# Performance work log

Measured on AMD Instinct MI355X. Metric: run time of the kernel, lower is better.

Reference implementation:

```python
import jax, jax.numpy as jnp
import numpy as np

B, T, E, H = 2, 2048, 1024, 16
HD = E // H
EPS = 1e-5


def layer_norm(x, g, b):
    mu = jnp.mean(x, axis=-1, keepdims=True)
    var = jnp.mean(jnp.square(x - mu), axis=-1, keepdims=True)
    return (x - mu) * jax.lax.rsqrt(var + EPS) * g + b


def setup_inputs() -> dict:
    key = jax.random.key(0)
    ks = jax.random.split(key, 12)
    s = 0.02
    return {
        "x": jax.random.normal(ks[0], (B, T, E), jnp.float32),
        "Wk": jax.random.normal(ks[1], (E, E), jnp.float32) * s,
        "Wq": jax.random.normal(ks[2], (E, E), jnp.float32) * s,
        "Wv": jax.random.normal(ks[3], (E, E), jnp.float32) * s,
        "Wp": jax.random.normal(ks[4], (E, E), jnp.float32) * s,
        "bp": jnp.zeros((E,), jnp.float32),
        "W1": jax.random.normal(ks[5], (E, 4 * E), jnp.float32) * s,
        "b1": jnp.zeros((4 * E,), jnp.float32),
        "W2": jax.random.normal(ks[6], (4 * E, E), jnp.float32) * s,
        "b2": jnp.zeros((E,), jnp.float32),
        "g1": jnp.ones((E,), jnp.float32),
        "be1": jnp.zeros((E,), jnp.float32),
        "g2": jnp.ones((E,), jnp.float32),
        "be2": jnp.zeros((E,), jnp.float32),
    }


def reference(x, Wk, Wq, Wv, Wp, bp, W1, b1, W2, b2, g1, be1, g2, be2):
    # --- attention sublayer ---
    h = layer_norm(x, g1, be1)
    q = (h @ Wq).reshape(B, T, H, HD).transpose(0, 2, 1, 3)  # [B,H,T,HD]
    k = (h @ Wk).reshape(B, T, H, HD).transpose(0, 2, 1, 3)
    v = (h @ Wv).reshape(B, T, H, HD).transpose(0, 2, 1, 3)
    scores = jnp.einsum('bhqd,bhkd->bhqk', q, k) * (HD ** -0.5)
    causal = jnp.tril(jnp.ones((T, T), bool))
    scores = jnp.where(causal, scores, -jnp.inf)
    probs = jax.nn.softmax(scores, axis=-1)  # dropout is identity (eval)
    attn = jnp.einsum('bhqk,bhkd->bhqd', probs, v)
    attn = attn.transpose(0, 2, 1, 3).reshape(B, T, E)
    x = x + attn @ Wp + bp
    # --- FFN sublayer ---
    h2 = layer_norm(x, g2, be2)
    ff = jax.nn.relu(h2 @ W1 + b1) @ W2 + b2
    return x + ff
```

## Files before the change

kernel.cpp:

```cpp
#include <hip/hip_runtime.h>
#include <hip/hip_bf16.h>

#define B_ 2
#define T_ 2048
#define E_ 1024
#define H_ 16
#define HD_ 64
#define NT (B_*T_)

typedef __attribute__((ext_vector_type(8))) short s16x8;
typedef __attribute__((ext_vector_type(4))) float f32x4;

using bf16 = __hip_bfloat16;

#define MFMA16(a,b,c) __builtin_amdgcn_mfma_f32_16x16x32_bf16(a,b,c,0,0,0)

__device__ inline unsigned short f2bf(float f) {
    bf16 h = __float2bfloat16(f);
    return *reinterpret_cast<unsigned short*>(&h);
}

__device__ __forceinline__ unsigned cvt_pk_bf16(float lo, float hi) {
    unsigned r;
    asm("v_cvt_pk_bf16_f32 %0, %1, %2" : "=v"(r) : "v"(lo), "v"(hi));
    return r;
}

__device__ __forceinline__ float exp2_fast(float x) {
    float r;
    asm("v_exp_f32 %0, %1" : "=v"(r) : "v"(x));
    return r;
}

__device__ __forceinline__ void async_cp16(const void* g, void* l) {
    __builtin_amdgcn_global_load_lds((const __attribute__((address_space(1))) void*)g,
                                     (__attribute__((address_space(3))) void*)l,
                                     16, 0, 0);
}

__global__ __launch_bounds__(256) void transpose_all(const float* __restrict__ Wq,
                                                     const float* __restrict__ Wk,
                                                     const float* __restrict__ Wv,
                                                     const float* __restrict__ Wp,
                                                     const float* __restrict__ W1,
                                                     const float* __restrict__ W2,
                                                     bf16* __restrict__ Wqkv_t,
                                                     bf16* __restrict__ W1_t,
                                                     bf16* __restrict__ W2_t) {
    __shared__ float tile[32][33];
    int id = blockIdx.x;
    const float* src; bf16* dst; int K, N, n0, k0;
    float scl = 1.0f;
    if (id < 4096) {
        int z = id >> 10, t = id & 1023;
        src = z == 0 ? Wq : z == 1 ? Wk : z == 2 ? Wv : Wp;
        if (z == 0) scl = 0.125f * 1.44269504088896f;
        dst = Wqkv_t + (size_t)z * 1048576;
        K = 1024; N = 1024; n0 = (t & 31) * 32; k0 = (t >> 5) * 32;
    } else if (id < 8192) {
        int t = id - 4096; src = W1; dst = W1_t; K = 1024; N = 4096;
        n0 = (t & 127) * 32; k0 = (t >> 7) * 32;
    } else {
        int t = id - 8192; src = W2; dst = W2_t; K = 4096; N = 1024;
        n0 = (t & 31) * 32; k0 = (t >> 5) * 32;
    }
    int tx = threadIdx.x, ty = threadIdx.y;
#pragma unroll
    for (int i = 0; i < 4; ++i)
        tile[ty + i*8][tx] = src[(size_t)(k0 + ty + i*8)*N + n0 + tx];
    __syncthreads();
#pragma unroll
    for (int i = 0; i < 4; ++i)
        dst[(size_t)(n0 + ty + i*8)*K + k0 + tx] = __float2bfloat16(tile[tx][ty + i*8] * scl);
}

__global__ __launch_bounds__(256) void ln_kernel(const float* __restrict__ x,
                                                 const float* __restrict__ g,
                                                 const float* __restrict__ b,
                                                 bf16* __restrict__ h) {
    int row = blockIdx.x;
    int tid = threadIdx.x;
    const float4 xv = *reinterpret_cast<const float4*>(x + (size_t)row*E_ + tid*4);
    float s  = xv.x + xv.y + xv.z + xv.w;
    float sq = xv.x*xv.x + xv.y*xv.y + xv.z*xv.z + xv.w*xv.w;
#pragma unroll
    for (int o = 32; o > 0; o >>= 1) { s += __shfl_xor(s, o); sq += __shfl_xor(sq, o); }
    __shared__ float red[8];
    int w = tid >> 6, lane = tid & 63;
    if (lane == 0) { red[w] = s; red[4 + w] = sq; }
    __syncthreads();
    float S = red[0] + red[1] + red[2] + red[3];
    float Q = red[4] + red[5] + red[6] + red[7];
    float mu = S * (1.0f/E_);
    float var = Q * (1.0f/E_) - mu*mu;
    float rs = rsqrtf(var + 1e-5f);
    const float4 gv = *reinterpret_cast<const float4*>(g + tid*4);
    const float4 bv = *reinterpret_cast<const float4*>(b + tid*4);
    ushort4 o4;
    o4.x = f2bf((xv.x - mu)*rs*gv.x + bv.x);
    o4.y = f2bf((xv.y - mu)*rs*gv.y + bv.y);
    o4.z = f2bf((xv.z - mu)*rs*gv.z + bv.z);
    o4.w = f2bf((xv.w - mu)*rs*gv.w + bv.w);
    *reinterpret_cast<ushort4*>(h + (size_t)row*E_ + tid*4) = o4;
}

#define RD(p) (*reinterpret_cast<const s16x8*>(p))
#define MM(m,n) do { acc[m][n] = MFMA16(af[m][0], bfr[n][0], acc[m][n]); \
                     acc[m][n] = MFMA16(af[m][1], bfr[n][1], acc[m][n]); } while (0)
#define MFMAS_0 MM(0,0); MM(1,0);
#define MFMAS_1 MM(2,0); MM(3,0); MM(2,1); MM(3,1); MM(0,1); MM(1,1);
#define MFMAS_2 MM(4,0); MM(5,0); MM(4,1); MM(5,1); MM(4,2); MM(5,2); \
                MM(0,2); MM(1,2); MM(2,2); MM(3,2);
#define MFMAS_3 MM(6,0); MM(7,0); MM(6,1); MM(7,1); MM(6,2); MM(7,2); \
                MM(6,3); MM(7,3); MM(0,3); MM(1,3); MM(2,3); MM(3,3); \
                MM(4,3); MM(5,3);

template<int EPI>
__global__ __launch_bounds__(512)
void gemm8p(const bf16* __restrict__ A, const bf16* __restrict__ Bt, void* Cout,
            const float* __restrict__ bias, int M, int N, int K) {
    __shared__ char smem[131072];
    int tid = threadIdx.x;
    int lane = tid & 63, w = tid >> 6;
    int wm = w >> 2, wn = w & 3;
    int nbx = gridDim.x;
    int hid = blockIdx.y * nbx + blockIdx.x;
    int cpx = (nbx * gridDim.y) >> 3;
    int nid = (hid & 7) * cpx + (hid >> 3);
    int m0 = (nid / nbx) * 256, n0 = (nid % nbx) * 256;
    int lr = lane & 15, lq = lane >> 4;
    f32x4 acc[8][4] = {};
    int srow = tid >> 3;
    int schunk = ((tid & 7) ^ (srow & 7)) * 8;
    const bf16* ApS = A  + (size_t)(m0 + srow)*K + schunk;
    const bf16* BpS = Bt + (size_t)(n0 + srow)*K + schunk;
    int sw4 = (lr & 7) << 4;
    int x0 = (lq*16) ^ sw4, x1 = (64 + lq*16) ^ sw4;
    int aoff[8], boff[4];
#pragma unroll
    for (int m = 0; m < 8; ++m)
        aoff[m] = ((m >> 1)*64 + wm*32 + (m & 1)*16 + lr) * 128;
#pragma unroll
    for (int n = 0; n < 4; ++n)
        boff[n] = (n*64 + wn*16 + lr) * 128;
    int nst = K >> 6;
    s16x8 af[8][2], bfr[4][2];
#pragma unroll
    for (int q = 0; q < 4; ++q) {
        async_cp16(ApS + (size_t)(q*64)*K, smem + q*8192 + w*1024);
        async_cp16(BpS + (size_t)(q*64)*K, smem + 32768 + q*8192 + w*1024);
    }
    ApS += 64; BpS += 64;
    asm volatile("s_waitcnt vmcnt(6)" ::: "memory");
    __builtin_amdgcn_sched_barrier(0);
    __builtin_amdgcn_s_barrier();
    __builtin_amdgcn_sched_barrier(0);

#define PHASE(Q) do {                                                              \
    af[2*Q][0]   = RD(bufA + aoff[2*Q]   + x0);                                    \
    af[2*Q][1]   = RD(bufA + aoff[2*Q]   + x1);                                    \
    af[2*Q+1][0] = RD(bufA + aoff[2*Q+1] + x0);                                    \
    af[2*Q+1][1] = RD(bufA + aoff[2*Q+1] + x1);                                    \
    bfr[Q][0]    = RD(bufB + boff[Q] + x0);                                        \
    bfr[Q][1]    = RD(bufB + boff[Q] + x1);                                        \
    if (more) {                                                                    \
        async_cp16(ApS + (size_t)(Q*64)*K, stA + Q*8192 + w*1024);                 \
        async_cp16(BpS + (size_t)(Q*64)*K, stA + 32768 + Q*8192 + w*1024);         \
        asm volatile("s_waitcnt vmcnt(6)" ::: "memory");                           \
    } else {                                                                       \
        if (Q == 0) asm volatile("s_waitcnt vmcnt(4)" ::: "memory");               \
        else if (Q == 1) asm volatile("s_waitcnt vmcnt(2)" ::: "memory");          \
        else if (Q == 2) asm volatile("s_waitcnt vmcnt(0)" ::: "memory");          \
    }                                                                              \
    __builtin_amdgcn_sched_barrier(0);                                             \
    __builtin_amdgcn_s_barrier();                                                  \
    __builtin_amdgcn_sched_barrier(0);                                             \
    asm volatile("s_waitcnt lgkmcnt(0)" ::: "memory");                             \
    __builtin_amdgcn_sched_barrier(0);                                             \
    __builtin_amdgcn_s_setprio(1);                                                 \
    MFMAS_##Q                                                                      \
    __builtin_amdgcn_s_setprio(0);                                                 \
    __builtin_amdgcn_sched_barrier(0);                                             \
    __builtin_amdgcn_s_barrier();                                                  \
    __builtin_amdgcn_sched_barrier(0);                                             \
} while (0)

    for (int t = 0; t < nst; ++t) {
        const char* bufA = smem + (size_t)(t & 1)*65536;
        const char* bufB = bufA + 32768;
        char* stA = smem + (size_t)((t & 1) ^ 1)*65536;
        bool more = (t + 1 < nst);
        PHASE(0);
        PHASE(1);
        PHASE(2);
        PHASE(3);
        ApS += 64; BpS += 64;
    }
#undef PHASE
#pragma unroll
    for (int m = 0; m < 8; ++m) {
#pragma unroll
        for (int n = 0; n < 4; ++n) {
            int col = n0 + n*64 + wn*16 + lr;
#pragma unroll
            for (int r = 0; r < 4; ++r) {
                int row = m0 + (m >> 1)*64 + wm*32 + (m & 1)*16 + lq*4 + r;
                float v = acc[m][n][r];
                if (EPI == 0) {
                    reinterpret_cast<bf16*>(Cout)[(size_t)row*N + col] = __float2bfloat16(v);
                } else {
                    v += bias[col];
                    v = v > 0.f ? v : 0.f;
                    reinterpret_cast<bf16*>(Cout)[(size_t)row*N + col] = __float2bfloat16(v);
                }
            }
        }
    }
}

template<int BM, int BN, int EPI>
__global__ __launch_bounds__(256)
void gemm_t(const bf16* __restrict__ A, const bf16* __restrict__ Bt, void* Cout,
            const float* __restrict__ bias, const float* res,
            int M, int N, int K) {
    constexpr int MT = BM / 32;
    constexpr int NB = BN / 32;
    constexpr int MHALF = BM / 2, NHALF = BN / 2;
    __shared__ bf16 As[BM*64];
    __shared__ bf16 Bs[BN*64];
    int tid = threadIdx.x;
    int lane = tid & 63, w = tid >> 6;
    int wr = w >> 1, wc = w & 1;
    int nbx = gridDim.x;
    int hid = blockIdx.y * nbx + blockIdx.x;
    int cpx = (nbx * gridDim.y) >> 3;
    int nid = (hid & 7) * cpx + (hid >> 3);
    int m0 = (nid / nbx) * BM, n0 = (nid % nbx) * BN;
    int lr = lane & 15, lq = lane >> 4;
    f32x4 acc[MT][NB] = {};
    int srow = w*8 + (lane >> 3);
    int schunk = ((lane & 7) ^ (srow & 7)) * 8;
    const bf16* Ap = A  + (size_t)(m0 + srow)*K + schunk;
    const bf16* Bp = Bt + (size_t)(n0 + srow)*K + schunk;
    for (int k0 = 0; k0 < K; k0 += 64) {
#pragma unroll
        for (int i = 0; i < BM/32; ++i)
            async_cp16(Ap + (size_t)(i*32)*K + k0, (char*)As + i*4096 + w*1024);
#pragma unroll
        for (int i = 0; i < BN/32; ++i)
            async_cp16(Bp + (size_t)(i*32)*K + k0, (char*)Bs + i*4096 + w*1024);
        __syncthreads();
        const char* Asb = (const char*)As;
        const char* Bsb = (const char*)Bs;
        s16x8 af[2][MT], bfr[2][NB];
#pragma unroll
        for (int m = 0; m < MT; ++m) {
            int row = wr*MHALF + m*16 + lr;
            int base = row*128, sw = (row & 7) << 4;
#pragma unroll
            for (int kk = 0; kk < 2; ++kk)
                af[kk][m] = *reinterpret_cast<const s16x8*>(Asb + base + ((kk*64 + lq*16) ^ sw));
        }
#pragma unroll
        for (int n = 0; n < NB; ++n) {
            int row = wc*NHALF + n*16 + lr;
            int base = row*128, sw = (row & 7) << 4;
#pragma unroll
            for (int kk = 0; kk < 2; ++kk)
                bfr[kk][n] = *reinterpret_cast<const s16x8*>(Bsb + base + ((kk*64 + lq*16) ^ sw));
        }
        __builtin_amdgcn_s_setprio(1);
#pragma unroll
        for (int kk = 0; kk < 2; ++kk)
#pragma unroll
            for (int m = 0; m < MT; ++m)
#pragma unroll
                for (int n = 0; n < NB; ++n)
                    acc[m][n] = MFMA16(af[kk][m], bfr[kk][n], acc[m][n]);
        __builtin_amdgcn_s_setprio(0);
        __syncthreads();
    }
#pragma unroll
    for (int m = 0; m < MT; ++m) {
#pragma unroll
        for (int n = 0; n < NB; ++n) {
            int col = n0 + wc*NHALF + n*16 + lr;
#pragma unroll
            for (int r = 0; r < 4; ++r) {
                int row = m0 + wr*MHALF + m*16 + lq*4 + r;
                float v = acc[m][n][r];
                if (EPI == 0) {
                    reinterpret_cast<bf16*>(Cout)[(size_t)row*N + col] = __float2bfloat16(v);
                } else if (EPI == 1) {
                    reinterpret_cast<float*>(Cout)[(size_t)row*N + col] =
                        v + bias[col] + res[(size_t)row*N + col];
                } else {
                    v += bias[col];
                    v = v > 0.f ? v : 0.f;
                    reinterpret_cast<bf16*>(Cout)[(size_t)row*N + col] = __float2bfloat16(v);
                }
            }
        }
    }
}

__global__ __launch_bounds__(256) void v_transpose(const bf16* __restrict__ qkv,
                                                   bf16* __restrict__ Vt) {
    __shared__ unsigned short tile[32][33];
    int tx = threadIdx.x, ty = threadIdx.y;
    int bh = blockIdx.z;
    int b = bh >> 4, h = bh & 15;
    int t0 = blockIdx.x * 32, d0 = blockIdx.y * 32;
    const unsigned short* src = reinterpret_cast<const unsigned short*>(qkv);
#pragma unroll
    for (int i = 0; i < 4; ++i)
        tile[ty + i*8][tx] = src[(size_t)(b*T_ + t0 + ty + i*8)*3072 + 2048 + h*64 + d0 + tx];
    __syncthreads();
    unsigned short* dst = reinterpret_cast<unsigned short*>(Vt);
#pragma unroll
    for (int i = 0; i < 4; ++i)
        dst[(size_t)(bh*64 + d0 + ty + i*8)*T_ + t0 + tx] = tile[tx][ty + i*8];
}

__global__ __launch_bounds__(256)
void flash_attn(const bf16* __restrict__ qkv, const bf16* __restrict__ Vt,
                bf16* __restrict__ O) {
    __shared__ char smem[40960];
    int tid = threadIdx.x;
    int lane = tid & 63, w = tid >> 6;
    int lr = lane & 15, lq = lane >> 4;
    int bh = blockIdx.y, b = bh >> 4, h = bh & 15;
    int pm = (bh & 15) ^ ((bh & 16) ? 31 : 0);
    int qt = (int)(blockIdx.x ^ pm) & 31;
    int q0 = qt * 64;
    int qw = q0 + w * 16;
    const bf16* Qb = qkv + (size_t)(b*T_)*3072 + h*HD_;
    const bf16* Kb = Qb + 1024;
    const bf16* Vb = Vt + (size_t)bh * HD_ * T_;
    char* Pw = smem + 32768 + w*2048;

    int srow_ = w*8 + (lane >> 3);
    int sc_   = (((lane & 7) ^ (srow_ & 7))) * 8;
    const bf16* kS0 = Kb + (size_t)srow_*3072 + sc_;
    const bf16* kS1 = kS0 + (size_t)32*3072;
    const bf16* vS0 = Vb + (size_t)srow_*2048 + sc_;
    const bf16* vS1 = vS0 + (size_t)32*2048;
    char* kD = smem + w*1024;
    char* vD = smem + 16384 + w*1024;

    int sw4 = (lr & 7) << 4;
    int kvo[4], pwo[4];
#pragma unroll
    for (int n = 0; n < 4; ++n) {
        kvo[n] = n*2048 + lr*128 + ((lq << 4) ^ sw4);
        pwo[n] = (lr*128 + n*32 + lq*8) ^ sw4;
    }
    int pao0 = (lr*128 + lq*16) ^ sw4;
    int pao1 = (lr*128 + 64 + lq*16) ^ sw4;

    s16x8 qf[2];
#pragma unroll
    for (int kk = 0; kk < 2; ++kk)
        qf[kk] = *reinterpret_cast<const s16x8*>(Qb + (size_t)(qw + lr)*3072 + kk*32 + lq*8);
    f32x4 od[4] = {};
    const f32x4 Z4 = {0.f, 0.f, 0.f, 0.f};
    float lrun = 0.f;
    int ntiles = qt + 1;

    auto stageNext = [&](int bufi) {
        async_cp16(kS0, kD + bufi*8192);
        async_cp16(kS1, kD + bufi*8192 + 4096);
        async_cp16(vS0, vD + bufi*8192);
        async_cp16(vS1, vD + bufi*8192 + 4096);
        kS0 += 64*3072; kS1 += 64*3072; vS0 += 64; vS1 += 64;
    };

    auto step = [&](const char* Kt, const char* Vtl, bool diag, int kv0) {
        f32x4 sc[4];
        __builtin_amdgcn_s_setprio(1);
#pragma unroll
        for (int n = 0; n < 4; ++n) {
            s16x8 kf0 = *reinterpret_cast<const s16x8*>(Kt + kvo[n]);
            s16x8 kf1 = *reinterpret_cast<const s16x8*>(Kt + (kvo[n] ^ 64));
            f32x4 z = MFMA16(kf0, qf[0], Z4);
            z = MFMA16(kf1, qf[1], z);
            sc[n] = z;
        }
        __builtin_amdgcn_s_setprio(0);
        if (diag) {
            int q = qw + lr;
#pragma unroll
            for (int n = 0; n < 4; ++n)
#pragma unroll
                for (int r = 0; r < 4; ++r)
                    if (kv0 + n*16 + lq*4 + r > q) sc[n][r] = -1e30f;
        }
        float psum = 0.f;
#pragma unroll
        for (int n = 0; n < 4; ++n) {
            float p0 = exp2_fast(sc[n][0]);
            float p1 = exp2_fast(sc[n][1]);
            float p2 = exp2_fast(sc[n][2]);
            float p3 = exp2_fast(sc[n][3]);
            psum += (p0 + p1) + (p2 + p3);
            uint2 pk;
            pk.x = cvt_pk_bf16(p0, p1);
            pk.y = cvt_pk_bf16(p2, p3);
            *reinterpret_cast<uint2*>(Pw + pwo[n]) = pk;
        }
        psum += __shfl_xor(psum, 16);
        psum += __shfl_xor(psum, 32);
        lrun += psum;
        asm volatile("" ::: "memory");
        s16x8 pa0 = *reinterpret_cast<const s16x8*>(Pw + pao0);
        s16x8 pa1 = *reinterpret_cast<const s16x8*>(Pw + pao1);
        __builtin_amdgcn_s_setprio(1);
#pragma unroll
        for (int nd = 0; nd < 4; ++nd) {
            s16x8 vf0 = *reinterpret_cast<const s16x8*>(Vtl + kvo[nd]);
            s16x8 vf1 = *reinterpret_cast<const s16x8*>(Vtl + (kvo[nd] ^ 64));
            od[nd] = MFMA16(pa0, vf0, od[nd]);
            od[nd] = MFMA16(pa1, vf1, od[nd]);
        }
        __builtin_amdgcn_s_setprio(0);
    };

    stageNext(0);
    for (int it = 0; it < ntiles - 1; ++it) {
        int curb = it & 1;
        stageNext(curb ^ 1);
        asm volatile("s_waitcnt vmcnt(4)" ::: "memory");
        __builtin_amdgcn_sched_barrier(0);
        __builtin_amdgcn_s_barrier();
        __builtin_amdgcn_sched_barrier(0);
        step(smem + curb*8192, smem + 16384 + curb*8192, false, 0);
        __builtin_amdgcn_sched_barrier(0);
        __builtin_amdgcn_s_barrier();
        __builtin_amdgcn_sched_barrier(0);
    }
    {
        int curb = (ntiles - 1) & 1;
        asm volatile("s_waitcnt vmcnt(0)" ::: "memory");
        __builtin_amdgcn_sched_barrier(0);
        __builtin_amdgcn_s_barrier();
        __builtin_amdgcn_sched_barrier(0);
        step(smem + curb*8192, smem + 16384 + curb*8192, true, (ntiles - 1) * 64);
    }
    float lR[4];
#pragma unroll
    for (int r = 0; r < 4; ++r) lR[r] = 1.0f / __shfl(lrun, lq*4 + r);
#pragma unroll
    for (int nd = 0; nd < 4; ++nd) {
#pragma unroll
        for (int r = 0; r < 4; ++r) {
            int row = qw + lq*4 + r;
            O[(size_t)(b*T_ + row)*E_ + h*HD_ + nd*16 + lr] = __float2bfloat16(od[nd][r] * lR[r]);
        }
    }
}

extern "C" void kernel_launch(void* const* d_in, const int* in_sizes, int n_in,
                              void* d_out, int out_size, void* d_ws, size_t ws_size,
                              hipStream_t stream) {
    const float* x   = (const float*)d_in[0];
    const float* Wk  = (const float*)d_in[1];
    const float* Wq  = (const float*)d_in[2];
    const float* Wv  = (const float*)d_in[3];
    const float* Wp  = (const float*)d_in[4];
    const float* bp  = (const float*)d_in[5];
    const float* W1  = (const float*)d_in[6];
    const float* b1  = (const float*)d_in[7];
    const float* W2  = (const float*)d_in[8];
    const float* b2  = (const float*)d_in[9];
    const float* g1  = (const float*)d_in[10];
    const float* be1 = (const float*)d_in[11];
    const float* g2  = (const float*)d_in[12];
    const float* be2 = (const float*)d_in[13];
    float* out = (float*)d_out;

    char* ws = (char*)d_ws;
    bf16* Wqkv_t = (bf16*)(ws + 0);
    bf16* Wp_t   = (bf16*)(ws + 6291456);
    bf16* W1_t   = (bf16*)(ws + 8388608);
    bf16* W2_t   = (bf16*)(ws + 16777216);
    bf16* h      = (bf16*)(ws + 25165824);
    bf16* qkv    = (bf16*)(ws + 33554432);
    bf16* Vt     = (bf16*)(ws + 58720256);
    bf16* attnO  = (bf16*)(ws + 67108864);
    bf16* ff1    = (bf16*)(ws + 33554432);
    float* x2    = (ws_size >= 92274688) ? (float*)(ws + 75497472) : out;

    dim3 tb(32, 8);
    transpose_all<<<12288, tb, 0, stream>>>(Wq, Wk, Wv, Wp, W1, W2, Wqkv_t, W1_t, W2_t);

    ln_kernel<<<NT, 256, 0, stream>>>(x, g1, be1, h);
    gemm8p<0><<<dim3(12, 16), 512, 0, stream>>>(h, Wqkv_t, qkv, nullptr, NT, 3072, 1024);
    v_transpose<<<dim3(64, 2, 32), tb, 0, stream>>>(qkv, Vt);
    flash_attn<<<dim3(32, 32), 256, 0, stream>>>(qkv, Vt, attnO);
    gemm_t<64,64,1><<<dim3(16, 64), 256, 0, stream>>>(attnO, Wp_t, x2, bp, x, NT, 1024, 1024);
    ln_kernel<<<NT, 256, 0, stream>>>(x2, g2, be2, h);
    gemm8p<2><<<dim3(16, 16), 512, 0, stream>>>(h, W1_t, ff1, b1, NT, 4096, 1024);
    gemm_t<64,64,1><<<dim3(16, 64), 256, 0, stream>>>(ff1, W2_t, out, b2, x2, NT, 1024, 4096);
}
```

Measured before the change: 202.3 us.

## Use K=128 tiles for projection GEMMs and store residual x2 in bf16

Replaces the 64x64 gemm_t used for the output projection and the FFN down-projection with gemm_k128, which stages 128-wide K slices into a 16-way swizzled LDS layout with precomputed offsets. This halves the number of barrier-separated K iterations. When the workspace is large enough, the intermediate residual x2 is written in bf16 instead of fp32, and a bf16-input layernorm reads it. That cuts memory traffic for the residual write and for both of its reads, at the cost of lost precision in the residual stream.

```diff
diff --git a/kernel.cpp b/kernel.cpp
--- a/kernel.cpp
+++ b/kernel.cpp
@@ -18,6 +18,11 @@
 __device__ inline unsigned short f2bf(float f) {
     bf16 h = __float2bfloat16(f);
     return *reinterpret_cast<unsigned short*>(&h);
+}
+
+__device__ __forceinline__ float bf2f(unsigned short u) {
+    unsigned x = ((unsigned)u) << 16;
+    return __uint_as_float(x);
 }
 
 __device__ __forceinline__ unsigned cvt_pk_bf16(float lo, float hi) {
@@ -102,6 +107,130 @@
     o4.z = f2bf((xv.z - mu)*rs*gv.z + bv.z);
     o4.w = f2bf((xv.w - mu)*rs*gv.w + bv.w);
     *reinterpret_cast<ushort4*>(h + (size_t)row*E_ + tid*4) = o4;
+}
+
+__global__ __launch_bounds__(256) void ln_kernel_b(const bf16* __restrict__ x,
+                                                   const float* __restrict__ g,
+                                                   const float* __restrict__ b,
+                                                   bf16* __restrict__ h) {
+    int row = blockIdx.x;
+    int tid = threadIdx.x;
+    ushort4 u4 = *reinterpret_cast<const ushort4*>(x + (size_t)row*E_ + tid*4);
+    float v0 = bf2f(u4.x), v1 = bf2f(u4.y), v2 = bf2f(u4.z), v3 = bf2f(u4.w);
+    float s  = v0 + v1 + v2 + v3;
+    float sq = v0*v0 + v1*v1 + v2*v2 + v3*v3;
+#pragma unroll
+    for (int o = 32; o > 0; o >>= 1) { s += __shfl_xor(s, o); sq += __shfl_xor(sq, o); }
+    __shared__ float red[8];
+    int w = tid >> 6, lane = tid & 63;
+    if (lane == 0) { red[w] = s; red[4 + w] = sq; }
+    __syncthreads();
+    float S = red[0] + red[1] + red[2] + red[3];
+    float Q = red[4] + red[5] + red[6] + red[7];
+    float mu = S * (1.0f/E_);
+    float var = Q * (1.0f/E_) - mu*mu;
+    float rs = rsqrtf(var + 1e-5f);
+    const float4 gv = *reinterpret_cast<const float4*>(g + tid*4);
+    const float4 bv = *reinterpret_cast<const float4*>(b + tid*4);
+    ushort4 o4;
+    o4.x = f2bf((v0 - mu)*rs*gv.x + bv.x);
+    o4.y = f2bf((v1 - mu)*rs*gv.y + bv.y);
+    o4.z = f2bf((v2 - mu)*rs*gv.z + bv.z);
+    o4.w = f2bf((v3 - mu)*rs*gv.w + bv.w);
+    *reinterpret_cast<ushort4*>(h + (size_t)row*E_ + tid*4) = o4;
+}
+
+template<int EPI>
+__global__ __launch_bounds__(256)
+void gemm_k128(const bf16* __restrict__ A, const bf16* __restrict__ Bt, void* Cout,
+               const float* __restrict__ bias, const void* res,
+               int M, int N, int K) {
+    __shared__ bf16 As[64*128];
+    __shared__ bf16 Bs[64*128];
+    int tid = threadIdx.x;
+    int lane = tid & 63, w = tid >> 6;
+    int wr = w >> 1, wc = w & 1;
+    int nbx = gridDim.x;
+    int hid = blockIdx.y * nbx + blockIdx.x;
+    int cpx = (nbx * gridDim.y) >> 3;
+    int nid = (hid & 7) * cpx + (hid >> 3);
+    int m0 = (nid / nbx) * 64, n0 = (nid % nbx) * 64;
+    int lr = lane & 15, lq = lane >> 4;
+    f32x4 acc[2][2] = {};
+    int srow = w*4 + (lane >> 4);
+    int schunk = ((lane & 15) ^ (srow & 15)) * 8;
+    const bf16* Ap = A  + (size_t)(m0 + srow)*K + schunk;
+    const bf16* Bp = Bt + (size_t)(n0 + srow)*K + schunk;
+    int aoff[2][4], boff[2][4];
+#pragma unroll
+    for (int m = 0; m < 2; ++m) {
+        int R = wr*32 + m*16 + lr;
+#pragma unroll
+        for (int kk = 0; kk < 4; ++kk)
+            aoff[m][kk] = R*256 + (((kk*4 + lq) ^ lr) << 4);
+    }
+#pragma unroll
+    for (int n = 0; n < 2; ++n) {
+        int R = wc*32 + n*16 + lr;
+#pragma unroll
+        for (int kk = 0; kk < 4; ++kk)
+            boff[n][kk] = R*256 + (((kk*4 + lq) ^ lr) << 4);
+    }
+    for (int k0 = 0; k0 < K; k0 += 128) {
+#pragma unroll
+        for (int i = 0; i < 4; ++i)
+            async_cp16(Ap + (size_t)(i*16)*K + k0, (char*)As + i*4096 + w*1024);
+#pragma unroll
+        for (int i = 0; i < 4; ++i)
+            async_cp16(Bp + (size_t)(i*16)*K + k0, (char*)Bs + i*4096 + w*1024);
+        __syncthreads();
+        const char* Asb = (const char*)As;
+        const char* Bsb = (const char*)Bs;
+        s16x8 af[4][2], bfr[4][2];
+#pragma unroll
+        for (int m = 0; m < 2; ++m)
+#pragma unroll
+            for (int kk = 0; kk < 4; ++kk)
+                af[kk][m] = *reinterpret_cast<const s16x8*>(Asb + aoff[m][kk]);
+#pragma unroll
+        for (int n = 0; n < 2; ++n)
+#pragma unroll
+            for (int kk = 0; kk < 4; ++kk)
+                bfr[kk][n] = *reinterpret_cast<const s16x8*>(Bsb + boff[n][kk]);
+        __builtin_amdgcn_s_setprio(1);
+#pragma unroll
+        for (int kk = 0; kk < 4; ++kk)
+#pragma unroll
+            for (int m = 0; m < 2; ++m)
+#pragma unroll
+                for (int n = 0; n < 2; ++n)
+                    acc[m][n] = MFMA16(af[kk][m], bfr[kk][n], acc[m][n]);
+        __builtin_amdgcn_s_setprio(0);
+        __syncthreads();
+    }
+#pragma unroll
+    for (int m = 0; m < 2; ++m) {
+#pragma unroll
+        for (int n = 0; n < 2; ++n) {
+            int col = n0 + wc*32 + n*16 + lr;
+#pragma unroll
+            for (int r = 0; r < 4; ++r) {
+                int row = m0 + wr*32 + m*16 + lq*4 + r;
+                size_t idx = (size_t)row*N + col;
+                float v = acc[m][n][r] + bias[col];
+                if (EPI == 1) {
+                    reinterpret_cast<float*>(Cout)[idx] =
+                        v + reinterpret_cast<const float*>(res)[idx];
+                } else if (EPI == 3) {
+                    reinterpret_cast<bf16*>(Cout)[idx] =
+                        __float2bfloat16(v + reinterpret_cast<const float*>(res)[idx]);
+                } else {
+                    reinterpret_cast<float*>(Cout)[idx] =
+                        v + bf2f(reinterpret_cast<const unsigned short*>(res)[idx]);
+                }
+            }
+        }
+    }
 }
 
 #define RD(p) (*reinterpret_cast<const s16x8*>(p))
@@ -218,92 +347,6 @@
     }
 }
 
-template<int BM, int BN, int EPI>
-__global__ __launch_bounds__(256)
-void gemm_t(const bf16* __restrict__ A, const bf16* __restrict__ Bt, void* Cout,
-            const float* __restrict__ bias, const float* res,
-            int M, int N, int K) {
-    constexpr int MT = BM / 32;
-    constexpr int NB = BN / 32;
-    constexpr int MHALF = BM / 2, NHALF = BN / 2;
-    __shared__ bf16 As[BM*64];
-    __shared__ bf16 Bs[BN*64];
-    int tid = threadIdx.x;
-    int lane = tid & 63, w = tid >> 6;
-    int wr = w >> 1, wc = w & 1;
-    int nbx = gridDim.x;
-    int hid = blockIdx.y * nbx + blockIdx.x;
-    int cpx = (nbx * gridDim.y) >> 3;
-    int nid = (hid & 7) * cpx + (hid >> 3);
-    int m0 = (nid / nbx) * BM, n0 = (nid % nbx) * BN;
-    int lr = lane & 15, lq = lane >> 4;
-    f32x4 acc[MT][NB] = {};
-    int srow = w*8 + (lane >> 3);
-    int schunk = ((lane & 7) ^ (srow & 7)) * 8;
-    const bf16* Ap = A  + (size_t)(m0 + srow)*K + schunk;
-    const bf16* Bp = Bt + (size_t)(n0 + srow)*K + schunk;
-    for (int k0 = 0; k0 < K; k0 += 64) {
-#pragma unroll
-        for (int i = 0; i < BM/32; ++i)
-            async_cp16(Ap + (size_t)(i*32)*K + k0, (char*)As + i*4096 + w*1024);
-#pragma unroll
-        for (int i = 0; i < BN/32; ++i)
-            async_cp16(Bp + (size_t)(i*32)*K + k0, (char*)Bs + i*4096 + w*1024);
-        __syncthreads();
-        const char* Asb = (const char*)As;
-        const char* Bsb = (const char*)Bs;
-        s16x8 af[2][MT], bfr[2][NB];
-#pragma unroll
-        for (int m = 0; m < MT; ++m) {
-            int row = wr*MHALF + m*16 + lr;
-            int base = row*128, sw = (row & 7) << 4;
-#pragma unroll
-            for (int kk = 0; kk < 2; ++kk)
-                af[kk][m] = *reinterpret_cast<const s16x8*>(Asb + base + ((kk*64 + lq*16) ^ sw));
-        }
-#pragma unroll
-        for (int n = 0; n < NB; ++n) {
-            int row = wc*NHALF + n*16 + lr;
-            int base = row*128, sw = (row & 7) << 4;
-#pragma unroll
-            for (int kk = 0; kk < 2; ++kk)
-                bfr[kk][n] = *reinterpret_cast<const s16x8*>(Bsb + base + ((kk*64 + lq*16) ^ sw));
-        }
-        __builtin_amdgcn_s_setprio(1);
-#pragma unroll
-        for (int kk = 0; kk < 2; ++kk)
-#pragma unroll
-            for (int m = 0; m < MT; ++m)
-#pragma unroll
-                for (int n = 0; n < NB; ++n)
-                    acc[m][n] = MFMA16(af[kk][m], bfr[kk][n], acc[m][n]);
-        __builtin_amdgcn_s_setprio(0);
-        __syncthreads();
-    }
-#pragma unroll
-    for (int m = 0; m < MT; ++m) {
-#pragma unroll
-        for (int n = 0; n < NB; ++n) {
-            int col = n0 + wc*NHALF + n*16 + lr;
-#pragma unroll
-            for (int r = 0; r < 4; ++r) {
-                int row = m0 + wr*MHALF + m*16 + lq*4 + r;
-                float v = acc[m][n][r];
-                if (EPI == 0) {
-                    reinterpret_cast<bf16*>(Cout)[(size_t)row*N + col] = __float2bfloat16(v);
-                } else if (EPI == 1) {
-                    reinterpret_cast<float*>(Cout)[(size_t)row*N + col] =
-                        v + bias[col] + res[(size_t)row*N + col];
-                } else {
-                    v += bias[col];
-                    v = v > 0.f ? v : 0.f;
-                    reinterpret_cast<bf16*>(Cout)[(size_t)row*N + col] = __float2bfloat16(v);
-                }
-            }
-        }
-    }
-}
-
 __global__ __launch_bounds__(256) void v_transpose(const bf16* __restrict__ qkv,
                                                    bf16* __restrict__ Vt) {
     __shared__ unsigned short tile[32][33];
@@ -488,7 +531,8 @@
     bf16* Vt     = (bf16*)(ws + 58720256);
     bf16* attnO  = (bf16*)(ws + 67108864);
     bf16* ff1    = (bf16*)(ws + 33554432);
-    float* x2    = (ws_size >= 92274688) ? (float*)(ws + 75497472) : out;
+    bool big = ws_size >= 83886080;
+    bf16* x2b = (bf16*)(ws + 75497472);
 
     dim3 tb(32, 8);
     transpose_all<<<12288, tb, 0, stream>>>(Wq, Wk, Wv, Wp, W1, W2, Wqkv_t, W1_t, W2_t);
@@ -497,8 +541,15 @@
     gemm8p<0><<<dim3(12, 16), 512, 0, stream>>>(h, Wqkv_t, qkv, nullptr, NT, 3072, 1024);
     v_transpose<<<dim3(64, 2, 32), tb, 0, stream>>>(qkv, Vt);
     flash_attn<<<dim3(32, 32), 256, 0, stream>>>(qkv, Vt, attnO);
-    gemm_t<64,64,1><<<dim3(16, 64), 256, 0, stream>>>(attnO, Wp_t, x2, bp, x, NT, 1024, 1024);
-    ln_kernel<<<NT, 256, 0, stream>>>(x2, g2, be2, h);
-    gemm8p<2><<<dim3(16, 16), 512, 0, stream>>>(h, W1_t, ff1, b1, NT, 4096, 1024);
-    gemm_t<64,64,1><<<dim3(16, 64), 256, 0, stream>>>(ff1, W2_t, out, b2, x2, NT, 1024, 4096);
-}
+    if (big) {
+        gemm_k128<3><<<dim3(16, 64), 256, 0, stream>>>(attnO, Wp_t, x2b, bp, x, NT, 1024, 1024);
+        ln_kernel_b<<<NT, 256, 0, stream>>>(x2b, g2, be2, h);
+        gemm8p<2><<<dim3(16, 16), 512, 0, stream>>>(h, W1_t, ff1, b1, NT, 4096, 1024);
+        gemm_k128<4><<<dim3(16, 64), 256, 0, stream>>>(ff1, W2_t, out, b2, x2b, NT, 1024, 4096);
+    } else {
+        gemm_k128<1><<<dim3(16, 64), 256, 0, stream>>>(attnO, Wp_t, out, bp, x, NT, 1024, 1024);
+        ln_kernel<<<NT, 256, 0, stream>>>(out, g2, be2, h);
+        gemm8p<2><<<dim3(16, 16), 512, 0, stream>>>(h, W1_t, ff1, b1, NT, 4096, 1024);
+        gemm_k128<1><<<dim3(16, 64), 256, 0, stream>>>(ff1, W2_t, out, b2, out, NT, 1024, 4096);
+    }
+}
```

New measurement: 204.8 us. About the same (+1.2%).
